# Optimization experiments

Measured on AMD Instinct MI355X. Metric: run time of the kernel, lower is better.

The kernel has to match this reference:

```python
import jax, jax.numpy as jnp
import numpy as np

HEADS = 16
DIM_HEAD = 64
SCALE = DIM_HEAD ** -0.5


def setup_inputs() -> dict:
    key = jax.random.key(0)
    ks = jax.random.split(key, 8)
    b, n, dim = 8, 4096, 1024
    inner = HEADS * DIM_HEAD
    return {
        "x": jax.random.normal(ks[0], (b, n, dim), dtype=jnp.float32),
        "mask": jnp.ones((b, n), dtype=bool),
        "W_qkv": jax.random.normal(ks[1], (dim, inner * 3), dtype=jnp.float32) * (dim ** -0.5),
        "w_q_logits": jax.random.normal(ks[2], (DIM_HEAD,), dtype=jnp.float32) * (DIM_HEAD ** -0.5),
        "w_k_logits": jax.random.normal(ks[3], (DIM_HEAD,), dtype=jnp.float32) * (DIM_HEAD ** -0.5),
        "W_r": jax.random.normal(ks[4], (DIM_HEAD, DIM_HEAD), dtype=jnp.float32) * (DIM_HEAD ** -0.5),
        "b_r": jnp.zeros((DIM_HEAD,), dtype=jnp.float32),
        "W_out": jax.random.normal(ks[5], (inner, dim), dtype=jnp.float32) * (inner ** -0.5),
        "b_out": jnp.zeros((dim,), dtype=jnp.float32),
    }


def reference(x, mask, W_qkv, w_q_logits, w_k_logits, W_r, b_r, W_out, b_out):
    b, n, dim = x.shape
    mask_value = -jnp.finfo(x.dtype).max
    qkv = x @ W_qkv  # [b, n, 3*inner]
    q, k, v = jnp.split(qkv, 3, axis=-1)
    # 'b n (h d) -> b h n d'
    split_heads = lambda t: t.reshape(b, n, HEADS, DIM_HEAD).transpose(0, 2, 1, 3)
    q, k, v = split_heads(q), split_heads(k), split_heads(v)
    m = mask[:, None, :]  # b 1 n

    # query attention logits: Linear(dim_head -> 1), scale, mask, softmax
    q_logits = jnp.einsum('bhnd,d->bhn', q, w_q_logits) * SCALE
    q_logits = jnp.where(m, q_logits, mask_value)
    q_attn = jax.nn.softmax(q_logits, axis=-1)
    global_q = jnp.einsum('bhn,bhnd->bhd', q_attn, q)  # aggr = q (no rotary)

    # gate keys with global query
    k_gated = k * global_q[:, :, None, :]
    k_logits = jnp.einsum('bhnd,d->bhn', k_gated, w_k_logits) * SCALE
    k_logits = jnp.where(m, k_logits, mask_value)
    k_attn = jax.nn.softmax(k_logits, axis=-1)
    global_k = jnp.einsum('bhn,bhnd->bhd', k_attn, k)

    # gate values with global key, project, residual with q
    u = v * global_k[:, :, None, :]
    r = u @ W_r + b_r + q  # [b, h, n, d]
    r = r.transpose(0, 2, 1, 3).reshape(b, n, HEADS * DIM_HEAD)
    return r @ W_out + b_out
```

## Files before the change

### kernel.cpp

```cpp
#include <hip/hip_runtime.h>


typedef unsigned short u16;
typedef unsigned int u32;
typedef __attribute__((ext_vector_type(8))) short short8;
typedef __attribute__((ext_vector_type(4))) float f32x4;
typedef __attribute__((ext_vector_type(4))) unsigned short us4;

#define SCALE_F 0.125f
#define NPART 33554432ull

static __device__ __forceinline__ float bf2f(u16 u) {
  union { u32 i; float f; } x; x.i = ((u32)u) << 16; return x.f;
}
static __device__ __forceinline__ u16 f2bf(float f) {
  u32 u = __float_as_uint(f);
  u += 0x7fffu + ((u >> 16) & 1u);
  return (u16)(u >> 16);
}

__global__ __launch_bounds__(256) void k_cvt(const float* __restrict__ in,
                                             u16* __restrict__ out) {
  int i = blockIdx.x * 256 + threadIdx.x;
  f32x4 v = ((const f32x4*)in)[i];
  us4 o;
  o[0] = f2bf(v[0]); o[1] = f2bf(v[1]); o[2] = f2bf(v[2]); o[3] = f2bf(v[3]);
  ((us4*)out)[i] = o;
}

__global__ __launch_bounds__(256) void k_transpose_cvt(const float* __restrict__ in,
                                                       u16* __restrict__ out,
                                                       int K, int N) {
  __shared__ float t[32][33];
  int kb = blockIdx.x * 32, nb = blockIdx.y * 32;
  int tx = threadIdx.x & 31, ty = threadIdx.x >> 5;
#pragma unroll
  for (int i = 0; i < 32; i += 8) t[ty + i][tx] = in[(size_t)(kb + ty + i) * N + nb + tx];
  __syncthreads();
#pragma unroll
  for (int i = 0; i < 32; i += 8)
    out[(size_t)(nb + ty + i) * K + kb + tx] = f2bf(t[tx][ty + i]);
}


#define AO(b, kh) ((b) * 16384 + (kh) * 8192)
#define BO(b, kh) (32768 + (b) * 16384 + (kh) * 8192)

#define STAGE(gb, roff, tau, kh) do {                                          \
    int t_ = (tau); if (t_ >= NT) t_ -= NT;                                    \
    size_t k0_ = (size_t)t_ * 64 + (kh) * 32;                                  \
    const u16* s0_ = (gb) + sgoff0 + k0_;                                      \
    __builtin_amdgcn_global_load_lds(                                          \
        (const __attribute__((address_space(1))) void*)s0_,                    \
        (__attribute__((address_space(3))) void*)(lds + (roff) + sldsW),       \
        16, 0, 0);                                                             \
    __builtin_amdgcn_global_load_lds(                                          \
        (const __attribute__((address_space(1))) void*)(s0_ + (size_t)128 * K),\
        (__attribute__((address_space(3))) void*)(lds + (roff) + 4096 + sldsW),\
        16, 0, 0);                                                             \
  } while (0)

#define PHASE(mh, kh, beta, STAGE_STMT, DO_WAIT) do {                          \
    const u16* ap_ = lds + AO(beta, kh) + (wm * 128 + (mh) * 64) * 32 + rAB;   \
    const u16* bp_ = lds + BO(beta, kh) + (wn * 64) * 32 + rAB;                \
    short8 av_[4], bv_[4];                                                     \
    _Pragma("unroll") for (int i_ = 0; i_ < 4; ++i_)                           \
      av_[i_] = *(const short8*)(ap_ + i_ * 512);                              \
    _Pragma("unroll") for (int n_ = 0; n_ < 4; ++n_)                           \
      bv_[n_] = *(const short8*)(bp_ + n_ * 512);                              \
    STAGE_STMT;                                                                \
    if (DO_WAIT) asm volatile("s_waitcnt vmcnt(6)" ::: "memory");              \
    __builtin_amdgcn_s_barrier();                                              \
    __builtin_amdgcn_s_setprio(1);                                             \
    _Pragma("unroll") for (int i_ = 0; i_ < 4; ++i_)                           \
      _Pragma("unroll") for (int n_ = 0; n_ < 4; ++n_)                         \
        acc[(mh) * 4 + i_][n_] = __builtin_amdgcn_mfma_f32_16x16x32_bf16(      \
            av_[i_], bv_[n_], acc[(mh) * 4 + i_][n_], 0, 0, 0);                \
    __builtin_amdgcn_s_setprio(0);                                             \
    __builtin_amdgcn_sched_barrier(0);                                         \
    __builtin_amdgcn_s_barrier();                                              \
    __builtin_amdgcn_sched_barrier(0);                                         \
  } while (0)

template <int EPI>
__global__ __launch_bounds__(512, 2) void k_gemm8(const u16* __restrict__ A,
                                                  const u16* __restrict__ BT,
                                                  void* __restrict__ Cout,
                                                  const float* __restrict__ bias,
                                                  int N, int K, int ntcol) {
  __shared__ u16 lds[65536];
  const int tid = threadIdx.x;
  const int wid = tid >> 6, lane = tid & 63;
  const int wm = wid >> 2, wn = wid & 3;

  int nwg = gridDim.x, chunkw = nwg >> 3, bid = blockIdx.x;
  int tile = (bid & 7) * chunkw + (bid >> 3);
  int rt = tile / ntcol, ct = tile - rt * ntcol;
  int row0 = rt * 256, col0 = ct * 256;

  const u16* Ab = A + (size_t)row0 * K;
  const u16* Bb = BT + (size_t)col0 * K;
  const int NT = K >> 6;

  const size_t sgoff0 = (size_t)(tid >> 2) * K +
                        (size_t)(((lane & 3) ^ ((lane >> 3) & 3)) * 8);
  const int sldsW = wid * 16 * 32;

  const int rAB = (lane & 15) * 32 + (((lane >> 4) ^ ((lane >> 1) & 3)) * 8);

  f32x4 acc[8][4];
#pragma unroll
  for (int m = 0; m < 8; ++m)
#pragma unroll
    for (int n = 0; n < 4; ++n) acc[m][n] = (f32x4){0.f, 0.f, 0.f, 0.f};

  STAGE(Ab, AO(0, 0), 0, 0);
  STAGE(Bb, BO(0, 0), 0, 0);
  STAGE(Ab, AO(0, 1), 0, 1);
  STAGE(Bb, BO(0, 1), 0, 1);
  STAGE(Ab, AO(1, 0), 1, 0);
  asm volatile("s_waitcnt vmcnt(6)" ::: "memory");
  __builtin_amdgcn_s_barrier();
  __builtin_amdgcn_sched_barrier(0);

  for (int g = 0; g < NT; g += 2) {
    PHASE(0, 0, 0, STAGE(Bb, BO(1, 0), g + 1, 0), 0);
    PHASE(1, 0, 0, STAGE(Ab, AO(1, 1), g + 1, 1), 1);
    PHASE(0, 1, 0, STAGE(Bb, BO(1, 1), g + 1, 1), 0);
    PHASE(1, 1, 0, STAGE(Ab, AO(0, 0), g + 2, 0), 1);
    PHASE(0, 0, 1, STAGE(Bb, BO(0, 0), g + 2, 0), 0);
    PHASE(1, 0, 1, STAGE(Ab, AO(0, 1), g + 2, 1), 1);
    PHASE(0, 1, 1, STAGE(Bb, BO(0, 1), g + 2, 1), 0);
    PHASE(1, 1, 1, STAGE(Ab, AO(1, 0), g + 3, 0), 1);
  }

  int cr = row0 + wm * 128 + ((lane >> 4) << 2);
  int cc = col0 + wn * 64 + (lane & 15);
  if (EPI == 0) {
    float* C = (float*)Cout;
#pragma unroll
    for (int m = 0; m < 8; ++m)
#pragma unroll
      for (int n = 0; n < 4; ++n)
#pragma unroll
        for (int r = 0; r < 4; ++r) {
          int row = cr + m * 16 + r, col = cc + n * 16;
          C[(size_t)row * N + col] = acc[m][n][r] + bias[col];
        }
  } else {
    int colw = col0 + wn * 64;
    u16* dst = (u16*)Cout + (size_t)(colw >> 10) * NPART;
    int h = (colw & 1023) >> 6;
#pragma unroll
    for (int m = 0; m < 8; ++m)
#pragma unroll
      for (int n = 0; n < 4; ++n)
#pragma unroll
        for (int r = 0; r < 4; ++r) {
          int row = cr + m * 16 + r;
          int d = n * 16 + (lane & 15);
          int b = row >> 12, nr = row & 4095;
          dst[((size_t)((b << 4) + h) * 4096 + nr) * 64 + d] = f2bf(acc[m][n][r]);
        }
  }
}

__global__ __launch_bounds__(256) void k_logits(const u16* __restrict__ X,
                                                const float* __restrict__ w, int perBH,
                                                float* __restrict__ out) {
  int chunk = blockIdx.x, bh = blockIdx.y;
  int t = threadIdx.x, lane = t & 63, wv = t >> 6;
  const float* wp = perBH ? w + bh * 64 : w;
  int sub = lane & 7, d0 = sub * 8;
  f32x4 w0 = *(const f32x4*)(wp + d0);
  f32x4 w1 = *(const f32x4*)(wp + d0 + 4);
  size_t base = (size_t)bh * 4096 + chunk * 128;
#pragma unroll
  for (int i = 0; i < 4; i++) {
    int row = wv * 32 + i * 8 + (lane >> 3);
    short8 xv = *(const short8*)(X + (base + row) * 64 + d0);
    float s = 0.f;
#pragma unroll
    for (int j = 0; j < 4; j++) s += bf2f((u16)xv[j]) * w0[j];
#pragma unroll
    for (int j = 0; j < 4; j++) s += bf2f((u16)xv[j + 4]) * w1[j];
    s += __shfl_xor(s, 1); s += __shfl_xor(s, 2); s += __shfl_xor(s, 4);
    if (sub == 0) out[base + row] = s * SCALE_F;
  }
}

__global__ __launch_bounds__(256) void k_ms(float* __restrict__ p,
                                            float* __restrict__ ms) {
  __shared__ float red[256];
  int bh = blockIdx.x, t = threadIdx.x;
  float* lg = p + (size_t)bh * 4096;
  float mx = -3.4e38f;
#pragma unroll
  for (int i = 0; i < 16; i++) mx = fmaxf(mx, lg[t + i * 256]);
  red[t] = mx; __syncthreads();
  for (int s = 128; s > 0; s >>= 1) { if (t < s) red[t] = fmaxf(red[t], red[t + s]); __syncthreads(); }
  float bm = red[0]; __syncthreads();
  float sum = 0.f;
#pragma unroll
  for (int i = 0; i < 16; i++) {
    float e = __expf(lg[t + i * 256] - bm);
    lg[t + i * 256] = e;
    sum += e;
  }
  red[t] = sum; __syncthreads();
  for (int s = 128; s > 0; s >>= 1) { if (t < s) red[t] += red[t + s]; __syncthreads(); }
  if (t == 0) ms[bh] = 1.f / red[0];
}

__global__ __launch_bounds__(256) void k_pool(const float* __restrict__ p,
                                              const u16* __restrict__ X,
                                              float* __restrict__ part) {
  __shared__ float sm[4][64];
  int chunk = blockIdx.x, bh = blockIdx.y;
  int t = threadIdx.x, d = t & 63, g = t >> 6;
  size_t base = (size_t)bh * 4096 + chunk * 128;
  float acc = 0.f;
#pragma unroll 8
  for (int i = 0; i < 32; i++) {
    int row = g * 32 + i;
    acc += p[base + row] * bf2f(X[(base + row) * 64 + d]);
  }
  sm[g][d] = acc; __syncthreads();
  if (t < 64) {
    float s = sm[0][t] + sm[1][t] + sm[2][t] + sm[3][t];
    part[((size_t)bh * 32 + chunk) * 64 + t] = s;
  }
}

__global__ __launch_bounds__(64) void k_final(const float* __restrict__ part,
                                              const float* __restrict__ ms,
                                              float* __restrict__ gout,
                                              const float* __restrict__ wk,
                                              float* __restrict__ weff) {
  int bh = blockIdx.x, d = threadIdx.x;
  float s = 0.f;
#pragma unroll 8
  for (int c = 0; c < 32; c++) s += part[((size_t)bh * 32 + c) * 64 + d];
  s *= ms[bh];
  gout[bh * 64 + d] = s;
  if (wk) weff[bh * 64 + d] = s * wk[d];
}

__global__ __launch_bounds__(256) void k_fuse_r(const u16* __restrict__ Vh,
                                                const u16* __restrict__ Qh,
                                                const float* __restrict__ gk,
                                                const float* __restrict__ Wr,
                                                const float* __restrict__ br,
                                                u16* __restrict__ rb) {
  __shared__ u16 Wsb[4096];
  int chunk = blockIdx.x, bh = blockIdx.y;
  int b = bh >> 4, h = bh & 15;
  int t = threadIdx.x, wid = t >> 6, lane = t & 63;

  {
    int d = t & 63;
    float g = gk[bh * 64 + d];
#pragma unroll
    for (int i = 0; i < 16; i++) {
      int dp = (t >> 6) + i * 4;
      u16 v = f2bf(g * Wr[d * 64 + dp]);
      *(u16*)((char*)Wsb + dp * 128 + (((u32)(d * 2)) ^ ((u32)(dp & 7) << 4))) = v;
    }
  }
  __syncthreads();

  size_t gvbase = (size_t)bh * 4096 + chunk * 128;
  short8 a[2][2], bfr[4][2];
#pragma unroll
  for (int m = 0; m < 2; m++)
#pragma unroll
    for (int kk = 0; kk < 2; kk++) {
      int row = wid * 32 + m * 16 + (lane & 15);
      int k = kk * 32 + ((lane >> 4) << 3);
      a[m][kk] = *(const short8*)(Vh + (gvbase + row) * 64 + k);
    }
#pragma unroll
  for (int n = 0; n < 4; n++)
#pragma unroll
    for (int kk = 0; kk < 2; kk++) {
      int dp = n * 16 + (lane & 15);
      u32 off = (u32)(kk * 64 + ((lane >> 4) << 4)) ^ ((u32)(dp & 7) << 4);
      bfr[n][kk] = *(const short8*)((const char*)Wsb + dp * 128 + off);
    }
  f32x4 zero = {0.f, 0.f, 0.f, 0.f};
  f32x4 acc[2][4];
#pragma unroll
  for (int m = 0; m < 2; m++)
#pragma unroll
    for (int n = 0; n < 4; n++) acc[m][n] = zero;
#pragma unroll
  for (int kk = 0; kk < 2; kk++)
#pragma unroll
    for (int m = 0; m < 2; m++)
#pragma unroll
      for (int n = 0; n < 4; n++)
        acc[m][n] = __builtin_amdgcn_mfma_f32_16x16x32_bf16(a[m][kk], bfr[n][kk], acc[m][n], 0, 0, 0);

#pragma unroll
  for (int m = 0; m < 2; m++)
#pragma unroll
    for (int n = 0; n < 4; n++)
#pragma unroll
      for (int r = 0; r < 4; r++) {
        int row = wid * 32 + m * 16 + ((lane >> 4) << 2) + r;
        int dp = n * 16 + (lane & 15);
        size_t grow = gvbase + row;
        float v = acc[m][n][r] + br[dp] + bf2f(Qh[grow * 64 + dp]);
        size_t mrow = (size_t)b * 4096 + chunk * 128 + row;
        rb[mrow * 1024 + h * 64 + dp] = f2bf(v);
      }
}

extern "C" void kernel_launch(void* const* d_in, const int* in_sizes, int n_in,
                              void* d_out, int out_size, void* d_ws, size_t ws_size,
                              hipStream_t stream) {
  (void)in_sizes; (void)n_in; (void)out_size; (void)ws_size;
  const float* x     = (const float*)d_in[0];
  const float* W_qkv = (const float*)d_in[2];
  const float* w_q   = (const float*)d_in[3];
  const float* w_k   = (const float*)d_in[4];
  const float* W_r   = (const float*)d_in[5];
  const float* b_r   = (const float*)d_in[6];
  const float* W_out = (const float*)d_in[7];
  const float* b_out = (const float*)d_in[8];

  char* ws = (char*)d_ws;
  u16*   xb    = (u16*)(ws + 0);
  u16*   rb    = (u16*)(ws + 0);
  u16*   wqkvT = (u16*)(ws + 67108864);
  u16*   woutT = (u16*)(ws + 73400320);
  u16*   QKVh  = (u16*)(ws + 75497472);
  u16*   Qh    = QKVh;
  u16*   Kh    = QKVh + NPART;
  u16*   Vh    = QKVh + 2 * NPART;
  float* p_buf = (float*)(ws + 67108864);
  float* partb = (float*)(ws + 69206016);
  float* ms    = (float*)(ws + 70254592);
  float* gq    = (float*)(ws + 70255104);
  float* gk    = (float*)(ws + 70287872);
  float* weff  = (float*)(ws + 70320640);

  k_cvt<<<32768, 256, 0, stream>>>(x, xb);
  k_transpose_cvt<<<dim3(32, 96), 256, 0, stream>>>(W_qkv, wqkvT, 1024, 3072);
  k_transpose_cvt<<<dim3(32, 32), 256, 0, stream>>>(W_out, woutT, 1024, 1024);

  k_gemm8<1><<<1536, 512, 0, stream>>>(xb, wqkvT, (void*)QKVh, nullptr,
                                       3072, 1024, 12);

  k_logits<<<dim3(32, 128), 256, 0, stream>>>(Qh, w_q, 0, p_buf);
  k_ms<<<128, 256, 0, stream>>>(p_buf, ms);
  k_pool<<<dim3(32, 128), 256, 0, stream>>>(p_buf, Qh, partb);
  k_final<<<128, 64, 0, stream>>>(partb, ms, gq, w_k, weff);

  k_logits<<<dim3(32, 128), 256, 0, stream>>>(Kh, weff, 1, p_buf);
  k_ms<<<128, 256, 0, stream>>>(p_buf, ms);
  k_pool<<<dim3(32, 128), 256, 0, stream>>>(p_buf, Kh, partb);
  k_final<<<128, 64, 0, stream>>>(partb, ms, gk, nullptr, nullptr);

  k_fuse_r<<<dim3(32, 128), 256, 0, stream>>>(Vh, Qh, gk, W_r, b_r, rb);

  k_gemm8<0><<<512, 512, 0, stream>>>(rb, woutT, d_out, b_out,
                                      1024, 1024, 4);
}
```

Baseline: 634.1 us.

## Fuse logits/softmax/pool into single-pass online-softmax kernel, stage GEMM epilogues via LDS

Replaces the four-kernel logits/max-sum/pool/final chain with one kernel per pass. Each block loads a 128-row chunk into LDS once, computes its logits, a local max and sum, and the exp-weighted pooled vector. A small combine kernel then merges the per-chunk results with a rescaled log-sum-exp. This drops one full re-read of Q/K and several launches. Separately, the GEMM epilogues now go through swizzled LDS so the global stores are coalesced 16-byte writes, and the main-loop barrier placement is reorganised to use one barrier per phase with the wait at its start. The risks are the extra LDS round-trip in the epilogue and the changed barrier and wait ordering in the pipelined loop.

```diff
diff --git a/kernel.cpp b/kernel.cpp
--- a/kernel.cpp
+++ b/kernel.cpp
@@ -60,7 +60,10 @@
         16, 0, 0);                                                             \
   } while (0)
 
-#define PHASE(mh, kh, beta, STAGE_STMT, DO_WAIT) do {                          \
+#define PHASE(mh, kh, beta, STAGE_STMT) do {                                   \
+    asm volatile("s_waitcnt vmcnt(6)" ::: "memory");                           \
+    __builtin_amdgcn_s_barrier();                                              \
+    __builtin_amdgcn_sched_barrier(0);                                         \
     const u16* ap_ = lds + AO(beta, kh) + (wm * 128 + (mh) * 64) * 32 + rAB;   \
     const u16* bp_ = lds + BO(beta, kh) + (wn * 64) * 32 + rAB;                \
     short8 av_[4], bv_[4];                                                     \
@@ -69,16 +72,12 @@
     _Pragma("unroll") for (int n_ = 0; n_ < 4; ++n_)                           \
       bv_[n_] = *(const short8*)(bp_ + n_ * 512);                              \
     STAGE_STMT;                                                                \
-    if (DO_WAIT) asm volatile("s_waitcnt vmcnt(6)" ::: "memory");              \
-    __builtin_amdgcn_s_barrier();                                              \
     __builtin_amdgcn_s_setprio(1);                                             \
     _Pragma("unroll") for (int i_ = 0; i_ < 4; ++i_)                           \
       _Pragma("unroll") for (int n_ = 0; n_ < 4; ++n_)                         \
         acc[(mh) * 4 + i_][n_] = __builtin_amdgcn_mfma_f32_16x16x32_bf16(      \
             av_[i_], bv_[n_], acc[(mh) * 4 + i_][n_], 0, 0, 0);                \
     __builtin_amdgcn_s_setprio(0);                                             \
-    __builtin_amdgcn_sched_barrier(0);                                         \
-    __builtin_amdgcn_s_barrier();                                              \
     __builtin_amdgcn_sched_barrier(0);                                         \
   } while (0)
 
@@ -119,131 +118,164 @@
   STAGE(Ab, AO(0, 1), 0, 1);
   STAGE(Bb, BO(0, 1), 0, 1);
   STAGE(Ab, AO(1, 0), 1, 0);
-  asm volatile("s_waitcnt vmcnt(6)" ::: "memory");
-  __builtin_amdgcn_s_barrier();
-  __builtin_amdgcn_sched_barrier(0);
 
   for (int g = 0; g < NT; g += 2) {
-    PHASE(0, 0, 0, STAGE(Bb, BO(1, 0), g + 1, 0), 0);
-    PHASE(1, 0, 0, STAGE(Ab, AO(1, 1), g + 1, 1), 1);
-    PHASE(0, 1, 0, STAGE(Bb, BO(1, 1), g + 1, 1), 0);
-    PHASE(1, 1, 0, STAGE(Ab, AO(0, 0), g + 2, 0), 1);
-    PHASE(0, 0, 1, STAGE(Bb, BO(0, 0), g + 2, 0), 0);
-    PHASE(1, 0, 1, STAGE(Ab, AO(0, 1), g + 2, 1), 1);
-    PHASE(0, 1, 1, STAGE(Bb, BO(0, 1), g + 2, 1), 0);
-    PHASE(1, 1, 1, STAGE(Ab, AO(1, 0), g + 3, 0), 1);
-  }
-
-  int cr = row0 + wm * 128 + ((lane >> 4) << 2);
-  int cc = col0 + wn * 64 + (lane & 15);
-  if (EPI == 0) {
-    float* C = (float*)Cout;
+    PHASE(0, 0, 0, STAGE(Bb, BO(1, 0), g + 1, 0));
+    PHASE(1, 0, 0, STAGE(Ab, AO(1, 1), g + 1, 1));
+    PHASE(0, 1, 0, STAGE(Bb, BO(1, 1), g + 1, 1));
+    PHASE(1, 1, 0, STAGE(Ab, AO(0, 0), g + 2, 0));
+    PHASE(0, 0, 1, STAGE(Bb, BO(0, 0), g + 2, 0));
+    PHASE(1, 0, 1, STAGE(Ab, AO(0, 1), g + 2, 1));
+    PHASE(0, 1, 1, STAGE(Bb, BO(0, 1), g + 2, 1));
+    PHASE(1, 1, 1, STAGE(Ab, AO(1, 0), g + 3, 0));
+  }
+
+  asm volatile("s_waitcnt vmcnt(0)" ::: "memory");
+  __syncthreads();
+
+  if (EPI == 1) {
+    u16* wl = lds + wid * 8192;
 #pragma unroll
     for (int m = 0; m < 8; ++m)
 #pragma unroll
       for (int n = 0; n < 4; ++n)
 #pragma unroll
         for (int r = 0; r < 4; ++r) {
-          int row = cr + m * 16 + r, col = cc + n * 16;
-          C[(size_t)row * N + col] = acc[m][n][r] + bias[col];
+          int row = m * 16 + ((lane >> 4) << 2) + r;
+          int col = n * 16 + (lane & 15);
+          wl[row * 64 + (col ^ ((row & 7) << 3))] = f2bf(acc[m][n][r]);
         }
+    __syncthreads();
+    int colW = col0 + wn * 64;
+    u16* dstW = (u16*)Cout + (size_t)(colW >> 10) * NPART +
+                ((size_t)(((row0 >> 12) << 4) + ((colW & 1023) >> 6)) * 4096 +
+                 (row0 & 4095) + wm * 128) * 64;
+#pragma unroll
+    for (int i = 0; i < 16; ++i) {
+      int row = i * 8 + (lane >> 3);
+      int c8 = (lane & 7) * 8;
+      short8 v = *(const short8*)(wl + row * 64 + (c8 ^ ((row & 7) << 3)));
+      *(short8*)(dstW + (size_t)row * 64 + c8) = v;
+    }
   } else {
-    int colw = col0 + wn * 64;
-    u16* dst = (u16*)Cout + (size_t)(colw >> 10) * NPART;
-    int h = (colw & 1023) >> 6;
-#pragma unroll
-    for (int m = 0; m < 8; ++m)
-#pragma unroll
-      for (int n = 0; n < 4; ++n)
-#pragma unroll
-        for (int r = 0; r < 4; ++r) {
-          int row = cr + m * 16 + r;
-          int d = n * 16 + (lane & 15);
-          int b = row >> 12, nr = row & 4095;
-          dst[((size_t)((b << 4) + h) * 4096 + nr) * 64 + d] = f2bf(acc[m][n][r]);
+    float* wlf = (float*)lds + wid * 4096;
+    float bcol[4];
+#pragma unroll
+    for (int n = 0; n < 4; ++n) bcol[n] = bias[col0 + wn * 64 + n * 16 + (lane & 15)];
+    float* Crow0 = (float*)Cout + (size_t)(row0 + wm * 128) * N + col0 + wn * 64;
+#pragma unroll
+    for (int half = 0; half < 2; ++half) {
+#pragma unroll
+      for (int m = 0; m < 8; ++m)
+#pragma unroll
+        for (int n2 = 0; n2 < 2; ++n2) {
+          int n = half * 2 + n2;
+#pragma unroll
+          for (int r = 0; r < 4; ++r) {
+            int row = m * 16 + ((lane >> 4) << 2) + r;
+            int col = n2 * 16 + (lane & 15);
+            wlf[row * 32 + (col ^ ((row & 7) << 2))] = acc[m][n][r] + bcol[n];
+          }
         }
-  }
-}
-
-__global__ __launch_bounds__(256) void k_logits(const u16* __restrict__ X,
-                                                const float* __restrict__ w, int perBH,
-                                                float* __restrict__ out) {
-  int chunk = blockIdx.x, bh = blockIdx.y;
-  int t = threadIdx.x, lane = t & 63, wv = t >> 6;
-  const float* wp = perBH ? w + bh * 64 : w;
-  int sub = lane & 7, d0 = sub * 8;
-  f32x4 w0 = *(const f32x4*)(wp + d0);
-  f32x4 w1 = *(const f32x4*)(wp + d0 + 4);
-  size_t base = (size_t)bh * 4096 + chunk * 128;
-#pragma unroll
-  for (int i = 0; i < 4; i++) {
-    int row = wv * 32 + i * 8 + (lane >> 3);
-    short8 xv = *(const short8*)(X + (base + row) * 64 + d0);
-    float s = 0.f;
-#pragma unroll
-    for (int j = 0; j < 4; j++) s += bf2f((u16)xv[j]) * w0[j];
-#pragma unroll
-    for (int j = 0; j < 4; j++) s += bf2f((u16)xv[j + 4]) * w1[j];
-    s += __shfl_xor(s, 1); s += __shfl_xor(s, 2); s += __shfl_xor(s, 4);
-    if (sub == 0) out[base + row] = s * SCALE_F;
-  }
-}
-
-__global__ __launch_bounds__(256) void k_ms(float* __restrict__ p,
-                                            float* __restrict__ ms) {
-  __shared__ float red[256];
-  int bh = blockIdx.x, t = threadIdx.x;
-  float* lg = p + (size_t)bh * 4096;
-  float mx = -3.4e38f;
-#pragma unroll
-  for (int i = 0; i < 16; i++) mx = fmaxf(mx, lg[t + i * 256]);
-  red[t] = mx; __syncthreads();
-  for (int s = 128; s > 0; s >>= 1) { if (t < s) red[t] = fmaxf(red[t], red[t + s]); __syncthreads(); }
-  float bm = red[0]; __syncthreads();
-  float sum = 0.f;
-#pragma unroll
-  for (int i = 0; i < 16; i++) {
-    float e = __expf(lg[t + i * 256] - bm);
-    lg[t + i * 256] = e;
-    sum += e;
-  }
-  red[t] = sum; __syncthreads();
-  for (int s = 128; s > 0; s >>= 1) { if (t < s) red[t] += red[t + s]; __syncthreads(); }
-  if (t == 0) ms[bh] = 1.f / red[0];
-}
-
-__global__ __launch_bounds__(256) void k_pool(const float* __restrict__ p,
-                                              const u16* __restrict__ X,
-                                              float* __restrict__ part) {
+      __syncthreads();
+      float* Crow = Crow0 + half * 32;
+#pragma unroll
+      for (int i = 0; i < 16; ++i) {
+        int row = i * 8 + (lane >> 3);
+        int c4 = (lane & 7) * 4;
+        f32x4 v = *(const f32x4*)(wlf + row * 32 + (c4 ^ ((row & 7) << 2)));
+        *(f32x4*)(Crow + (size_t)row * N + c4) = v;
+      }
+      __syncthreads();
+    }
+  }
+}
+
+__global__ __launch_bounds__(256) void k_attn_pool(const u16* __restrict__ X,
+                                                   const float* __restrict__ w,
+                                                   int perBH,
+                                                   float* __restrict__ pooled,
+                                                   float* __restrict__ Mc,
+                                                   float* __restrict__ Sc) {
+  __shared__ float Xs[128][65];
+  __shared__ float wl[64];
+  __shared__ float ex[128];
+  __shared__ float red[128];
   __shared__ float sm[4][64];
   int chunk = blockIdx.x, bh = blockIdx.y;
-  int t = threadIdx.x, d = t & 63, g = t >> 6;
-  size_t base = (size_t)bh * 4096 + chunk * 128;
+  int t = threadIdx.x;
+  size_t base = ((size_t)bh * 4096 + chunk * 128) * 64;
+  {
+    int row = t >> 3, c8 = (t & 7) * 8;
+#pragma unroll
+    for (int i = 0; i < 4; ++i) {
+      short8 v = *(const short8*)(X + base + (size_t)(row + i * 32) * 64 + c8);
+#pragma unroll
+      for (int j = 0; j < 8; ++j) Xs[row + i * 32][c8 + j] = bf2f((u16)v[j]);
+    }
+  }
+  if (t < 64) wl[t] = perBH ? w[bh * 64 + t] : w[t];
+  __syncthreads();
+  float lg = 0.f;
+  if (t < 128) {
+    float s = 0.f;
+#pragma unroll 16
+    for (int d = 0; d < 64; ++d) s += Xs[t][d] * wl[d];
+    lg = s * SCALE_F;
+    red[t] = lg;
+  }
+  __syncthreads();
+#pragma unroll
+  for (int s = 64; s > 0; s >>= 1) {
+    if (t < s) red[t] = fmaxf(red[t], red[t + s]);
+    __syncthreads();
+  }
+  float M_c = red[0];
+  __syncthreads();
+  if (t < 128) {
+    float e = __expf(lg - M_c);
+    ex[t] = e;
+    red[t] = e;
+  }
+  __syncthreads();
+#pragma unroll
+  for (int s = 64; s > 0; s >>= 1) {
+    if (t < s) red[t] += red[t + s];
+    __syncthreads();
+  }
+  float S_c = red[0];
+  int d = t & 63, g = t >> 6;
   float acc = 0.f;
 #pragma unroll 8
-  for (int i = 0; i < 32; i++) {
-    int row = g * 32 + i;
-    acc += p[base + row] * bf2f(X[(base + row) * 64 + d]);
-  }
-  sm[g][d] = acc; __syncthreads();
+  for (int i = 0; i < 32; ++i) acc += ex[g * 32 + i] * Xs[g * 32 + i][d];
+  sm[g][d] = acc;
+  __syncthreads();
   if (t < 64) {
-    float s = sm[0][t] + sm[1][t] + sm[2][t] + sm[3][t];
-    part[((size_t)bh * 32 + chunk) * 64 + t] = s;
-  }
-}
-
-__global__ __launch_bounds__(64) void k_final(const float* __restrict__ part,
-                                              const float* __restrict__ ms,
-                                              float* __restrict__ gout,
-                                              const float* __restrict__ wk,
-                                              float* __restrict__ weff) {
+    pooled[((size_t)bh * 32 + chunk) * 64 + t] = sm[0][t] + sm[1][t] + sm[2][t] + sm[3][t];
+    if (t == 0) { Mc[bh * 32 + chunk] = M_c; Sc[bh * 32 + chunk] = S_c; }
+  }
+}
+
+__global__ __launch_bounds__(64) void k_final2(const float* __restrict__ pooled,
+                                               const float* __restrict__ Mc,
+                                               const float* __restrict__ Sc,
+                                               float* __restrict__ gout,
+                                               const float* __restrict__ wk,
+                                               float* __restrict__ weff) {
   int bh = blockIdx.x, d = threadIdx.x;
-  float s = 0.f;
+  float M = -3.4e38f;
 #pragma unroll 8
-  for (int c = 0; c < 32; c++) s += part[((size_t)bh * 32 + c) * 64 + d];
-  s *= ms[bh];
-  gout[bh * 64 + d] = s;
-  if (wk) weff[bh * 64 + d] = s * wk[d];
+  for (int c = 0; c < 32; ++c) M = fmaxf(M, Mc[bh * 32 + c]);
+  float S = 0.f, P = 0.f;
+#pragma unroll 8
+  for (int c = 0; c < 32; ++c) {
+    float f = __expf(Mc[bh * 32 + c] - M);
+    S += Sc[bh * 32 + c] * f;
+    P += pooled[((size_t)bh * 32 + c) * 64 + d] * f;
+  }
+  float gv = P / S;
+  gout[bh * 64 + d] = gv;
+  if (wk) weff[bh * 64 + d] = gv * wk[d];
 }
 
 __global__ __launch_bounds__(256) void k_fuse_r(const u16* __restrict__ Vh,
@@ -256,7 +288,6 @@
   int chunk = blockIdx.x, bh = blockIdx.y;
   int b = bh >> 4, h = bh & 15;
   int t = threadIdx.x, wid = t >> 6, lane = t & 63;
-
   {
     int d = t & 63;
     float g = gk[bh * 64 + d];
@@ -300,7 +331,6 @@
 #pragma unroll
       for (int n = 0; n < 4; n++)
         acc[m][n] = __builtin_amdgcn_mfma_f32_16x16x32_bf16(a[m][kk], bfr[n][kk], acc[m][n], 0, 0, 0);
-
 #pragma unroll
   for (int m = 0; m < 2; m++)
 #pragma unroll
@@ -330,20 +360,20 @@
   const float* b_out = (const float*)d_in[8];
 
   char* ws = (char*)d_ws;
-  u16*   xb    = (u16*)(ws + 0);
-  u16*   rb    = (u16*)(ws + 0);
-  u16*   wqkvT = (u16*)(ws + 67108864);
-  u16*   woutT = (u16*)(ws + 73400320);
-  u16*   QKVh  = (u16*)(ws + 75497472);
-  u16*   Qh    = QKVh;
-  u16*   Kh    = QKVh + NPART;
-  u16*   Vh    = QKVh + 2 * NPART;
-  float* p_buf = (float*)(ws + 67108864);
-  float* partb = (float*)(ws + 69206016);
-  float* ms    = (float*)(ws + 70254592);
-  float* gq    = (float*)(ws + 70255104);
-  float* gk    = (float*)(ws + 70287872);
-  float* weff  = (float*)(ws + 70320640);
+  u16*   xb     = (u16*)(ws + 0);
+  u16*   rb     = (u16*)(ws + 0);
+  u16*   wqkvT  = (u16*)(ws + 67108864);
+  u16*   woutT  = (u16*)(ws + 73400320);
+  u16*   QKVh   = (u16*)(ws + 75497472);
+  u16*   Qh     = QKVh;
+  u16*   Kh     = QKVh + NPART;
+  u16*   Vh     = QKVh + 2 * NPART;
+  float* pooled = (float*)(ws + 67108864);
+  float* Mc     = (float*)(ws + 68157440);
+  float* Sc     = (float*)(ws + 68173824);
+  float* gq     = (float*)(ws + 68190208);
+  float* gk     = (float*)(ws + 68222976);
+  float* weff   = (float*)(ws + 68255744);
 
   k_cvt<<<32768, 256, 0, stream>>>(x, xb);
   k_transpose_cvt<<<dim3(32, 96), 256, 0, stream>>>(W_qkv, wqkvT, 1024, 3072);
@@ -352,15 +382,11 @@
   k_gemm8<1><<<1536, 512, 0, stream>>>(xb, wqkvT, (void*)QKVh, nullptr,
                                        3072, 1024, 12);
 
-  k_logits<<<dim3(32, 128), 256, 0, stream>>>(Qh, w_q, 0, p_buf);
-  k_ms<<<128, 256, 0, stream>>>(p_buf, ms);
-  k_pool<<<dim3(32, 128), 256, 0, stream>>>(p_buf, Qh, partb);
-  k_final<<<128, 64, 0, stream>>>(partb, ms, gq, w_k, weff);
-
-  k_logits<<<dim3(32, 128), 256, 0, stream>>>(Kh, weff, 1, p_buf);
-  k_ms<<<128, 256, 0, stream>>>(p_buf, ms);
-  k_pool<<<dim3(32, 128), 256, 0, stream>>>(p_buf, Kh, partb);
-  k_final<<<128, 64, 0, stream>>>(partb, ms, gk, nullptr, nullptr);
+  k_attn_pool<<<dim3(32, 128), 256, 0, stream>>>(Qh, w_q, 0, pooled, Mc, Sc);
+  k_final2<<<128, 64, 0, stream>>>(pooled, Mc, Sc, gq, w_k, weff);
+
+  k_attn_pool<<<dim3(32, 128), 256, 0, stream>>>(Kh, weff, 1, pooled, Mc, Sc);
+  k_final2<<<128, 64, 0, stream>>>(pooled, Mc, Sc, gk, nullptr, nullptr);
 
   k_fuse_r<<<dim3(32, 128), 256, 0, stream>>>(Vh, Qh, gk, W_r, b_r, rb);
 
```

Result: no change. 636.6 us (+0.4%).
